# Optimization experiments

Measured on AMD Instinct MI355X. Metric: run time of the kernel, lower is better.

Reference implementation:

```python
import jax, jax.numpy as jnp
import numpy as np

N = 10000   # nodes
E = 160000  # edges
D = 512     # input feat
H = 512     # hidden
O = 128     # output


def setup_inputs() -> dict:
    key = jax.random.key(0)
    ks = jax.random.split(key, 12)
    s = 0.05  # weight init scale
    inp = {
        "x": jax.random.normal(ks[0], (N, D), jnp.float32),
        "edge_index": jax.random.randint(ks[1], (2, E), 0, N, dtype=jnp.int64),
        "w_l0": jax.random.normal(ks[2], (D, H), jnp.float32) * s,
        "b_l0": jnp.zeros((H,), jnp.float32),
        "w_r0": jax.random.normal(ks[3], (D, H), jnp.float32) * s,
        "w_l1": jax.random.normal(ks[4], (H, H), jnp.float32) * s,
        "b_l1": jnp.zeros((H,), jnp.float32),
        "w_r1": jax.random.normal(ks[5], (H, H), jnp.float32) * s,
        "w_l2": jax.random.normal(ks[6], (H, H), jnp.float32) * s,
        "b_l2": jnp.zeros((H,), jnp.float32),
        "w_r2": jax.random.normal(ks[7], (H, H), jnp.float32) * s,
        "w_out": jax.random.normal(ks[8], (H, O), jnp.float32) * s,
        "b_out": jnp.zeros((O,), jnp.float32),
    }
    return inp


def _sage_conv(x, src, dst, w_l, b_l, w_r):
    # mean-aggregate source features at destination nodes (PyG SAGEConv, aggr='mean')
    agg = jax.ops.segment_sum(x[src], dst, num_segments=N)          # [N, d]
    deg = jax.ops.segment_sum(jnp.ones((src.shape[0], 1), x.dtype), dst, num_segments=N)
    agg = agg / jnp.maximum(deg, 1.0)
    # out = lin_l(agg) + lin_r(x_root)
    return agg @ w_l + b_l + x @ w_r


def reference(x, edge_index, w_l0, b_l0, w_r0, w_l1, b_l1, w_r1,
              w_l2, b_l2, w_r2, w_out, b_out):
    src, dst = edge_index[0], edge_index[1]
    x = jax.nn.relu(_sage_conv(x, src, dst, w_l0, b_l0, w_r0))
    x = jax.nn.relu(_sage_conv(x, src, dst, w_l1, b_l1, w_r1))
    x = jax.nn.relu(_sage_conv(x, src, dst, w_l2, b_l2, w_r2))
    return x @ w_out + b_out  # [N, O]
```

## Files before the change

kernel.cpp:

```cpp
#include <hip/hip_runtime.h>
#include <hip/hip_bf16.h>

#define KDIM 512
#define INIT_NBLK 512
#define INIT_GST (INIT_NBLK * 256)

typedef _Float16 f16x8 __attribute__((ext_vector_type(8)));
typedef float f32x4 __attribute__((ext_vector_type(4)));
typedef unsigned short u16x8 __attribute__((ext_vector_type(8)));

static __device__ __forceinline__ unsigned short f2h(float v) {
    _Float16 h = (_Float16)v;
    return *reinterpret_cast<unsigned short*>(&h);
}
static __device__ __forceinline__ float h2f(unsigned short u) {
    _Float16 h = *reinterpret_cast<_Float16*>(&u);
    return (float)h;
}


struct InitArgs {
    const float* x;
    const float* w[6];
    const float* wout;
    int* deg;
    unsigned short* xh;
    unsigned short* WT[3];
    unsigned short* WoT;
    int N, O;
};

__global__ __launch_bounds__(256) void init_kernel(InitArgs a) {
    __shared__ float tc[32][33];
    int b = blockIdx.x;
    int tid = threadIdx.x;
    int gtid = b * 256 + tid;

    for (int i = gtid; i < a.N; i += INIT_GST) a.deg[i] = 0;

    int total8 = a.N * (KDIM / 8);
    for (int i = gtid; i < total8; i += INIT_GST) {
        const float4* p = (const float4*)(a.x + (size_t)i * 8);
        float4 v0 = p[0], v1 = p[1];
        u16x8 h;
        h[0] = f2h(v0.x); h[1] = f2h(v0.y); h[2] = f2h(v0.z); h[3] = f2h(v0.w);
        h[4] = f2h(v1.x); h[5] = f2h(v1.y); h[6] = f2h(v1.z); h[7] = f2h(v1.w);
        *(u16x8*)(a.xh + (size_t)i * 8) = h;
    }

    int tx = tid & 31, ty = tid >> 5;
    for (int v = b; v < 1600; v += INIT_NBLK) {
        const float* W; unsigned short* T; int k0, n0, ldw;
        if (v < 1536) {
            int li = v >> 8;
            int t16 = v & 255;
            k0 = (t16 >> 4) * 32; n0 = (t16 & 15) * 32;
            W = a.w[li]; ldw = 512;
            T = a.WT[li >> 1] + (size_t)(li & 1) * 512 * KDIM;
        } else {
            int t2 = v - 1536;
            k0 = (t2 >> 2) * 32; n0 = (t2 & 3) * 32;
            W = a.wout; ldw = a.O; T = a.WoT;
        }
        __syncthreads();
#pragma unroll
        for (int j = 0; j < 4; ++j) {
            int r = ty + j * 8;
            tc[r][tx] = W[(size_t)(k0 + r) * ldw + n0 + tx];
        }
        __syncthreads();
#pragma unroll
        for (int j = 0; j < 4; ++j) {
            int rn = ty + j * 8;
            T[(size_t)(n0 + rn) * KDIM + k0 + tx] = f2h(tc[tx][rn]);
        }
    }
}


__global__ void deg_kernel(const int* __restrict__ dst, int* __restrict__ deg, int E) {
    int e = blockIdx.x * blockDim.x + threadIdx.x;
    if (e < E) atomicAdd(&deg[dst[e]], 1);
}

__global__ void scan_kernel(const int* __restrict__ deg, int* __restrict__ off, int n) {
    __shared__ int wsum[16];
    __shared__ int carry;
    int tid = threadIdx.x;
    int lane = tid & 63, wv = tid >> 6;
    if (tid == 0) carry = 0;
    __syncthreads();
    for (int start = 0; start < n; start += 1024) {
        int i = start + tid;
        int orig = (i < n) ? deg[i] : 0;
        int v = orig;
#pragma unroll
        for (int d = 1; d < 64; d <<= 1) {
            int t = __shfl_up(v, d, 64);
            if (lane >= d) v += t;
        }
        if (lane == 63) wsum[wv] = v;
        __syncthreads();
        int base = carry;
        if (wv == 0 && lane < 16) {
            int s = wsum[lane];
#pragma unroll
            for (int d = 1; d < 16; d <<= 1) {
                int t = __shfl_up(s, d, 64);
                if (lane >= d) s += t;
            }
            wsum[lane] = s;
            if (lane == 15) carry = base + s;
        }
        __syncthreads();
        int wpre = (wv == 0) ? 0 : wsum[wv - 1];
        if (i < n) off[i] = base + wpre + v - orig;
        __syncthreads();
    }
    if (tid == 0) off[n] = carry;
}

__global__ void fill_csr(const int* __restrict__ src, const int* __restrict__ dst,
                         const int* __restrict__ off, int* __restrict__ deg,
                         int* __restrict__ csr, int E) {
    int e = blockIdx.x * blockDim.x + threadIdx.x;
    if (e < E) {
        int d = dst[e];
        int p = atomicSub(&deg[d], 1);
        csr[off[d] + p - 1] = src[e];
    }
}


template<int BM, int BN, bool OUTBF>
__global__ __launch_bounds__(256) void gemm_mfma(
    const unsigned short* __restrict__ A, const unsigned short* __restrict__ B,
    const float* __restrict__ bias, float* __restrict__ outF,
    unsigned short* __restrict__ outB, int M, int ldo, int NBY, int relu) {
    constexpr int FM = BM / 32;
    constexpr int FN = BN / 32;
    __shared__ unsigned short As[BM * 64];
    __shared__ unsigned short Bs[BN * 64];

    int tid = threadIdx.x;
    int lane = tid & 63;
    int wid = tid >> 6;

    int nwg = gridDim.x;
    int q = nwg >> 3, rres = nwg & 7;
    int xcd = blockIdx.x & 7;
    int tile = (xcd < rres ? xcd * (q + 1) : rres * (q + 1) + (xcd - rres) * q)
             + (blockIdx.x >> 3);
    int rowBase = (tile / NBY) * BM;
    int colBase = (tile % NBY) * BN;

    int wm = (wid >> 1) * (BM / 2);
    int wn = (wid & 1) * (BN / 2);

    f32x4 acc[FM][FN] = {};

    int srow = lane >> 3;
    int scol = ((lane & 7) ^ srow) * 8;

    for (int kt = 0; kt < 8; ++kt) {
        int k0 = kt * 64;

#pragma unroll
        for (int s = 0; s < BM / 32; ++s) {
            int r0 = wid * (BM / 4) + s * 8;
            int gr = rowBase + r0 + srow;
            if (gr >= M) gr = M - 1;
            const unsigned short* g = A + (size_t)gr * KDIM + k0 + scol;
            __builtin_amdgcn_global_load_lds(
                (const __attribute__((address_space(1))) unsigned int*)g,
                (__attribute__((address_space(3))) unsigned int*)&As[r0 * 64],
                16, 0, 0);
        }
#pragma unroll
        for (int s = 0; s < BN / 32; ++s) {
            int r0 = wid * (BN / 4) + s * 8;
            const unsigned short* g = B + (size_t)(colBase + r0 + srow) * KDIM + k0 + scol;
            __builtin_amdgcn_global_load_lds(
                (const __attribute__((address_space(1))) unsigned int*)g,
                (__attribute__((address_space(3))) unsigned int*)&Bs[r0 * 64],
                16, 0, 0);
        }
        __syncthreads();

#pragma unroll
        for (int kk = 0; kk < 2; ++kk) {
            f16x8 aF[FM], bF[FN];
#pragma unroll
            for (int m = 0; m < FM; ++m) {
                int rr = wm + m * 16 + (lane & 15);
                int slot = ((kk << 2) + (lane >> 4)) ^ (lane & 7);
                aF[m] = *(const f16x8*)&As[rr * 64 + slot * 8];
            }
#pragma unroll
            for (int n = 0; n < FN; ++n) {
                int rn = wn + n * 16 + (lane & 15);
                int slot = ((kk << 2) + (lane >> 4)) ^ (lane & 7);
                bF[n] = *(const f16x8*)&Bs[rn * 64 + slot * 8];
            }
#pragma unroll
            for (int m = 0; m < FM; ++m)
#pragma unroll
                for (int n = 0; n < FN; ++n)
                    acc[m][n] = __builtin_amdgcn_mfma_f32_16x16x32_f16(aF[m], bF[n], acc[m][n], 0, 0, 0);
        }
        __syncthreads();
    }

#pragma unroll
    for (int n = 0; n < FN; ++n) {
        int col = colBase + wn + n * 16 + (lane & 15);
        float bb = bias ? bias[col] : 0.0f;
#pragma unroll
        for (int m = 0; m < FM; ++m) {
            int row0 = rowBase + wm + m * 16 + (lane >> 4) * 4;
#pragma unroll
            for (int r = 0; r < 4; ++r) {
                int row = row0 + r;
                if (row < M) {
                    float v = acc[m][n][r] + bb;
                    if (relu) v = fmaxf(v, 0.f);
                    if (OUTBF) outB[(size_t)row * ldo + col] = f2h(v);
                    else       outF[(size_t)row * ldo + col] = v;
                }
            }
        }
    }
}


__global__ __launch_bounds__(256) void gather_slice(
    const unsigned short* __restrict__ P, const int* __restrict__ off,
    const int* __restrict__ csr, const float* __restrict__ bias,
    unsigned short* __restrict__ oh, int n) {
    int slice = blockIdx.x & 7;
    int chunk = blockIdx.x >> 3;
    int wv = threadIdx.x >> 6;
    int lane = threadIdx.x & 63;
    int node = chunk * 4 + wv;
    if (node >= n) return;

    int esub = lane >> 3;
    int c8 = slice * 64 + (lane & 7) * 8;

    int beg = off[node], end = off[node + 1];
    float a[8] = {0.f, 0.f, 0.f, 0.f, 0.f, 0.f, 0.f, 0.f};
    int it = beg + esub;
    for (; it + 8 < end; it += 16) {
        int s0 = csr[it];
        int s1 = csr[it + 8];
        u16x8 v0 = *(const u16x8*)(P + (size_t)s0 * 1024 + c8);
        u16x8 v1 = *(const u16x8*)(P + (size_t)s1 * 1024 + c8);
#pragma unroll
        for (int j = 0; j < 8; ++j) a[j] += h2f(v0[j]) + h2f(v1[j]);
    }
    if (it < end) {
        int s0 = csr[it];
        u16x8 v0 = *(const u16x8*)(P + (size_t)s0 * 1024 + c8);
#pragma unroll
        for (int j = 0; j < 8; ++j) a[j] += h2f(v0[j]);
    }
#pragma unroll
    for (int j = 0; j < 8; ++j) {
        a[j] += __shfl_xor(a[j], 8);
        a[j] += __shfl_xor(a[j], 16);
        a[j] += __shfl_xor(a[j], 32);
    }

    if (esub == 0) {
        float inv = 1.0f / fmaxf((float)(end - beg), 1.0f);
        u16x8 p2 = *(const u16x8*)(P + (size_t)node * 1024 + 512 + c8);
        const float4* pb = (const float4*)(bias + c8);
        float4 b0 = pb[0], b1 = pb[1];
        float bbv[8] = {b0.x, b0.y, b0.z, b0.w, b1.x, b1.y, b1.z, b1.w};
        u16x8 h8;
#pragma unroll
        for (int j = 0; j < 8; ++j) {
            float v = fmaxf(a[j] * inv + h2f(p2[j]) + bbv[j], 0.f);
            h8[j] = f2h(v);
        }
        *(u16x8*)(oh + (size_t)node * KDIM + c8) = h8;
    }
}


extern "C" void kernel_launch(void* const* d_in, const int* in_sizes, int n_in,
                              void* d_out, int out_size, void* d_ws, size_t ws_size,
                              hipStream_t stream) {
    const float* x    = (const float*)d_in[0];
    const int*   ei   = (const int*)d_in[1];
    const float* bl0  = (const float*)d_in[3];
    const float* bl1  = (const float*)d_in[6];
    const float* bl2  = (const float*)d_in[9];
    const float* bout = (const float*)d_in[12];

    int N = in_sizes[0] / KDIM;
    int E = in_sizes[1] / 2;
    int O = in_sizes[12];

    const int* src = ei;
    const int* dst = ei + E;

    char* ws = (char*)d_ws;
    auto align = [](size_t o) { return (o + 255) & ~(size_t)255; };
    size_t o = 0;
    int* deg = (int*)(ws + o); o = align(o + (size_t)N * 4);
    int* off = (int*)(ws + o); o = align(o + (size_t)(N + 1) * 4);
    int* csr = (int*)(ws + o); o = align(o + (size_t)E * 4);

    size_t planeB = (size_t)N * KDIM * 2;
    unsigned short* x_h = (unsigned short*)(ws + o); o = align(o + planeB);
    unsigned short* a_h = (unsigned short*)(ws + o); o = align(o + planeB);
    unsigned short* P = (unsigned short*)(ws + o); o = align(o + (size_t)N * 1024 * 2);

    unsigned short* WT[3];
    for (int i = 0; i < 3; ++i) {
        WT[i] = (unsigned short*)(ws + o);
        o = align(o + (size_t)1024 * KDIM * 2);
    }
    unsigned short* WoT = (unsigned short*)(ws + o); o = align(o + (size_t)O * KDIM * 2);

    {
        InitArgs a;
        a.x = x;
        a.w[0] = (const float*)d_in[2];
        a.w[1] = (const float*)d_in[4];
        a.w[2] = (const float*)d_in[5];
        a.w[3] = (const float*)d_in[7];
        a.w[4] = (const float*)d_in[8];
        a.w[5] = (const float*)d_in[10];
        a.wout = (const float*)d_in[11];
        a.deg = deg;
        a.xh = x_h;
        for (int i = 0; i < 3; ++i) a.WT[i] = WT[i];
        a.WoT = WoT;
        a.N = N; a.O = O;
        init_kernel<<<INIT_NBLK, 256, 0, stream>>>(a);
    }

    deg_kernel<<<(E + 255) / 256, 256, 0, stream>>>(dst, deg, E);
    scan_kernel<<<1, 1024, 0, stream>>>(deg, off, N);
    fill_csr<<<(E + 255) / 256, 256, 0, stream>>>(src, dst, off, deg, csr, E);

    int nwgH = ((N + 63) / 64) * 8;
    int gatherBlocks = ((N + 3) / 4) * 8;
    const float* bl[3] = {bl0, bl1, bl2};
    unsigned short* inH[4] = {x_h, a_h, x_h, a_h};

    for (int i = 0; i < 3; ++i) {
        gemm_mfma<64, 128, true><<<nwgH, 256, 0, stream>>>(
            inH[i], WT[i], nullptr, nullptr, P, N, 1024, 8, 0);
        gather_slice<<<gatherBlocks, 256, 0, stream>>>(P, off, csr, bl[i], inH[i + 1], N);
    }

    {
        int nwgO = ((N + 63) / 64) * (O / 64);
        gemm_mfma<64, 64, false><<<nwgO, 256, 0, stream>>>(
            inH[3], WoT, bout, (float*)d_out, nullptr, N, O, O / 64, 0);
    }
}
```

Before: 311.3 us.

## Specialize GEMMs with 2-wave hidden tile and fp16 packed gather accumulation

Splits the templated GEMM into a dedicated hidden-layer kernel using 128 threads, where each wave covers all 64 rows and a 64-column slice, plus a separate output GEMM. The hidden GEMM's tile-to-XCD mapping drops the remainder handling, which assumes the block count is a multiple of 8. The gather now accumulates neighbour features in packed fp16 vectors and shuffles packed halves, cutting conversion and shuffle instructions. Accumulating in fp16 risks precision loss and overflow for high-degree nodes.

New measurement: 290.1 us. 1.07x faster.

```diff
diff --git a/kernel.cpp b/kernel.cpp
--- a/kernel.cpp
+++ b/kernel.cpp
@@ -132,42 +132,33 @@
 }
 
 
-template<int BM, int BN, bool OUTBF>
-__global__ __launch_bounds__(256) void gemm_mfma(
+__global__ __launch_bounds__(128) void gemm_h(
     const unsigned short* __restrict__ A, const unsigned short* __restrict__ B,
-    const float* __restrict__ bias, float* __restrict__ outF,
-    unsigned short* __restrict__ outB, int M, int ldo, int NBY, int relu) {
-    constexpr int FM = BM / 32;
-    constexpr int FN = BN / 32;
-    __shared__ unsigned short As[BM * 64];
-    __shared__ unsigned short Bs[BN * 64];
+    unsigned short* __restrict__ outB, int M) {
+    __shared__ unsigned short As[64 * 64];
+    __shared__ unsigned short Bs[128 * 64];
 
     int tid = threadIdx.x;
     int lane = tid & 63;
     int wid = tid >> 6;
 
     int nwg = gridDim.x;
-    int q = nwg >> 3, rres = nwg & 7;
-    int xcd = blockIdx.x & 7;
-    int tile = (xcd < rres ? xcd * (q + 1) : rres * (q + 1) + (xcd - rres) * q)
-             + (blockIdx.x >> 3);
-    int rowBase = (tile / NBY) * BM;
-    int colBase = (tile % NBY) * BN;
-
-    int wm = (wid >> 1) * (BM / 2);
-    int wn = (wid & 1) * (BN / 2);
-
-    f32x4 acc[FM][FN] = {};
+    int q = nwg >> 3;
+    int tile = (blockIdx.x & 7) * q + (blockIdx.x >> 3);
+    int rowBase = (tile >> 3) * 64;
+    int colBase = (tile & 7) * 128;
+    int wn = wid * 64;
+
+    f32x4 acc[4][4] = {};
 
     int srow = lane >> 3;
     int scol = ((lane & 7) ^ srow) * 8;
 
     for (int kt = 0; kt < 8; ++kt) {
         int k0 = kt * 64;
-
-#pragma unroll
-        for (int s = 0; s < BM / 32; ++s) {
-            int r0 = wid * (BM / 4) + s * 8;
+#pragma unroll
+        for (int s = 0; s < 4; ++s) {
+            int r0 = wid * 32 + s * 8;
             int gr = rowBase + r0 + srow;
             if (gr >= M) gr = M - 1;
             const unsigned short* g = A + (size_t)gr * KDIM + k0 + scol;
@@ -177,8 +168,8 @@
                 16, 0, 0);
         }
 #pragma unroll
-        for (int s = 0; s < BN / 32; ++s) {
-            int r0 = wid * (BN / 4) + s * 8;
+        for (int s = 0; s < 8; ++s) {
+            int r0 = wid * 64 + s * 8;
             const unsigned short* g = B + (size_t)(colBase + r0 + srow) * KDIM + k0 + scol;
             __builtin_amdgcn_global_load_lds(
                 (const __attribute__((address_space(1))) unsigned int*)g,
@@ -189,44 +180,121 @@
 
 #pragma unroll
         for (int kk = 0; kk < 2; ++kk) {
-            f16x8 aF[FM], bF[FN];
-#pragma unroll
-            for (int m = 0; m < FM; ++m) {
-                int rr = wm + m * 16 + (lane & 15);
-                int slot = ((kk << 2) + (lane >> 4)) ^ (lane & 7);
-                aF[m] = *(const f16x8*)&As[rr * 64 + slot * 8];
-            }
-#pragma unroll
-            for (int n = 0; n < FN; ++n) {
-                int rn = wn + n * 16 + (lane & 15);
-                int slot = ((kk << 2) + (lane >> 4)) ^ (lane & 7);
-                bF[n] = *(const f16x8*)&Bs[rn * 64 + slot * 8];
-            }
-#pragma unroll
-            for (int m = 0; m < FM; ++m)
-#pragma unroll
-                for (int n = 0; n < FN; ++n)
+            int slot = ((kk << 2) + (lane >> 4)) ^ (lane & 7);
+            f16x8 aF[4], bF[4];
+#pragma unroll
+            for (int m = 0; m < 4; ++m)
+                aF[m] = *(const f16x8*)&As[(m * 16 + (lane & 15)) * 64 + slot * 8];
+#pragma unroll
+            for (int n = 0; n < 4; ++n)
+                bF[n] = *(const f16x8*)&Bs[(wn + n * 16 + (lane & 15)) * 64 + slot * 8];
+#pragma unroll
+            for (int m = 0; m < 4; ++m)
+#pragma unroll
+                for (int n = 0; n < 4; ++n)
                     acc[m][n] = __builtin_amdgcn_mfma_f32_16x16x32_f16(aF[m], bF[n], acc[m][n], 0, 0, 0);
         }
         __syncthreads();
     }
 
 #pragma unroll
-    for (int n = 0; n < FN; ++n) {
+    for (int n = 0; n < 4; ++n) {
         int col = colBase + wn + n * 16 + (lane & 15);
-        float bb = bias ? bias[col] : 0.0f;
-#pragma unroll
-        for (int m = 0; m < FM; ++m) {
-            int row0 = rowBase + wm + m * 16 + (lane >> 4) * 4;
+#pragma unroll
+        for (int m = 0; m < 4; ++m) {
+            int row0 = rowBase + m * 16 + (lane >> 4) * 4;
 #pragma unroll
             for (int r = 0; r < 4; ++r) {
                 int row = row0 + r;
-                if (row < M) {
-                    float v = acc[m][n][r] + bb;
-                    if (relu) v = fmaxf(v, 0.f);
-                    if (OUTBF) outB[(size_t)row * ldo + col] = f2h(v);
-                    else       outF[(size_t)row * ldo + col] = v;
-                }
+                if (row < M)
+                    outB[(size_t)row * 1024 + col] = f2h(acc[m][n][r]);
+            }
+        }
+    }
+}
+
+
+__global__ __launch_bounds__(256) void gemm_out(
+    const unsigned short* __restrict__ A, const unsigned short* __restrict__ B,
+    const float* __restrict__ bias, float* __restrict__ outF, int M, int O) {
+    constexpr int BM = 64, BN = 64;
+    __shared__ unsigned short As[BM * 64];
+    __shared__ unsigned short Bs[BN * 64];
+
+    int tid = threadIdx.x;
+    int lane = tid & 63;
+    int wid = tid >> 6;
+
+    int nwg = gridDim.x;
+    int q = nwg >> 3, rres = nwg & 7;
+    int xcd = blockIdx.x & 7;
+    int tile = (xcd < rres ? xcd * (q + 1) : rres * (q + 1) + (xcd - rres) * q)
+             + (blockIdx.x >> 3);
+    int rowBase = (tile >> 1) * BM;
+    int colBase = (tile & 1) * BN;
+
+    int wm = (wid >> 1) * 32;
+    int wn = (wid & 1) * 32;
+
+    f32x4 acc[2][2] = {};
+    int srow = lane >> 3;
+    int scol = ((lane & 7) ^ srow) * 8;
+
+    for (int kt = 0; kt < 8; ++kt) {
+        int k0 = kt * 64;
+#pragma unroll
+        for (int s = 0; s < 2; ++s) {
+            int r0 = wid * 16 + s * 8;
+            int gr = rowBase + r0 + srow;
+            if (gr >= M) gr = M - 1;
+            const unsigned short* g = A + (size_t)gr * KDIM + k0 + scol;
+            __builtin_amdgcn_global_load_lds(
+                (const __attribute__((address_space(1))) unsigned int*)g,
+                (__attribute__((address_space(3))) unsigned int*)&As[r0 * 64],
+                16, 0, 0);
+        }
+#pragma unroll
+        for (int s = 0; s < 2; ++s) {
+            int r0 = wid * 16 + s * 8;
+            const unsigned short* g = B + (size_t)(colBase + r0 + srow) * KDIM + k0 + scol;
+            __builtin_amdgcn_global_load_lds(
+                (const __attribute__((address_space(1))) unsigned int*)g,
+                (__attribute__((address_space(3))) unsigned int*)&Bs[r0 * 64],
+                16, 0, 0);
+        }
+        __syncthreads();
+
+#pragma unroll
+        for (int kk = 0; kk < 2; ++kk) {
+            int slot = ((kk << 2) + (lane >> 4)) ^ (lane & 7);
+            f16x8 aF[2], bF[2];
+#pragma unroll
+            for (int m = 0; m < 2; ++m)
+                aF[m] = *(const f16x8*)&As[(wm + m * 16 + (lane & 15)) * 64 + slot * 8];
+#pragma unroll
+            for (int n = 0; n < 2; ++n)
+                bF[n] = *(const f16x8*)&Bs[(wn + n * 16 + (lane & 15)) * 64 + slot * 8];
+#pragma unroll
+            for (int m = 0; m < 2; ++m)
+#pragma unroll
+                for (int n = 0; n < 2; ++n)
+                    acc[m][n] = __builtin_amdgcn_mfma_f32_16x16x32_f16(aF[m], bF[n], acc[m][n], 0, 0, 0);
+        }
+        __syncthreads();
+    }
+
+#pragma unroll
+    for (int n = 0; n < 2; ++n) {
+        int col = colBase + wn + n * 16 + (lane & 15);
+        float bb = bias[col];
+#pragma unroll
+        for (int m = 0; m < 2; ++m) {
+            int row0 = rowBase + wm + m * 16 + (lane >> 4) * 4;
+#pragma unroll
+            for (int r = 0; r < 4; ++r) {
+                int row = row0 + r;
+                if (row < M)
+                    outF[(size_t)row * O + col] = acc[m][n][r] + bb;
             }
         }
     }
@@ -248,27 +316,27 @@
     int c8 = slice * 64 + (lane & 7) * 8;
 
     int beg = off[node], end = off[node + 1];
-    float a[8] = {0.f, 0.f, 0.f, 0.f, 0.f, 0.f, 0.f, 0.f};
+    f16x8 acc8 = {};
     int it = beg + esub;
     for (; it + 8 < end; it += 16) {
         int s0 = csr[it];
         int s1 = csr[it + 8];
-        u16x8 v0 = *(const u16x8*)(P + (size_t)s0 * 1024 + c8);
-        u16x8 v1 = *(const u16x8*)(P + (size_t)s1 * 1024 + c8);
-#pragma unroll
-        for (int j = 0; j < 8; ++j) a[j] += h2f(v0[j]) + h2f(v1[j]);
+        f16x8 v0 = *(const f16x8*)(P + (size_t)s0 * 1024 + c8);
+        f16x8 v1 = *(const f16x8*)(P + (size_t)s1 * 1024 + c8);
+        acc8 += v0 + v1;
     }
     if (it < end) {
         int s0 = csr[it];
-        u16x8 v0 = *(const u16x8*)(P + (size_t)s0 * 1024 + c8);
-#pragma unroll
-        for (int j = 0; j < 8; ++j) a[j] += h2f(v0[j]);
-    }
-#pragma unroll
-    for (int j = 0; j < 8; ++j) {
-        a[j] += __shfl_xor(a[j], 8);
-        a[j] += __shfl_xor(a[j], 16);
-        a[j] += __shfl_xor(a[j], 32);
+        acc8 += *(const f16x8*)(P + (size_t)s0 * 1024 + c8);
+    }
+#pragma unroll
+    for (int st = 8; st <= 32; st <<= 1) {
+        f16x8 other;
+        int* op = reinterpret_cast<int*>(&other);
+        const int* ap = reinterpret_cast<const int*>(&acc8);
+#pragma unroll
+        for (int w = 0; w < 4; ++w) op[w] = __shfl_xor(ap[w], st);
+        acc8 += other;
     }
 
     if (esub == 0) {
@@ -280,7 +348,7 @@
         u16x8 h8;
 #pragma unroll
         for (int j = 0; j < 8; ++j) {
-            float v = fmaxf(a[j] * inv + h2f(p2[j]) + bbv[j], 0.f);
+            float v = fmaxf((float)acc8[j] * inv + h2f(p2[j]) + bbv[j], 0.f);
             h8[j] = f2h(v);
         }
         *(u16x8*)(oh + (size_t)node * KDIM + c8) = h8;
@@ -352,14 +420,12 @@
     unsigned short* inH[4] = {x_h, a_h, x_h, a_h};
 
     for (int i = 0; i < 3; ++i) {
-        gemm_mfma<64, 128, true><<<nwgH, 256, 0, stream>>>(
-            inH[i], WT[i], nullptr, nullptr, P, N, 1024, 8, 0);
+        gemm_h<<<nwgH, 128, 0, stream>>>(inH[i], WT[i], P, N);
         gather_slice<<<gatherBlocks, 256, 0, stream>>>(P, off, csr, bl[i], inH[i + 1], N);
     }
 
     {
         int nwgO = ((N + 63) / 64) * (O / 64);
-        gemm_mfma<64, 64, false><<<nwgO, 256, 0, stream>>>(
-            inH[3], WoT, bout, (float*)d_out, nullptr, N, O, O / 64, 0);
-    }
-}
+        gemm_out<<<nwgO, 256, 0, stream>>>(inH[3], WoT, bout, (float*)d_out, N, O);
+    }
+}
```
